# Optimization experiments

Measured on AMD Instinct MI355X. Metric: run time of the kernel, lower is better.

## Reference

```python
import jax, jax.numpy as jnp
import numpy as np

V, D, N, S = 100000, 256, 8192, 20
H = D  # hidden size == feat_dim (nn.LSTM(feat_dim, feat_dim))


def setup_inputs() -> dict:
    key = jax.random.key(0)
    ks = jax.random.split(key, 8)
    sc = 1.0 / np.sqrt(H)  # PyTorch LSTM default init scale
    return {
        "emb": jax.random.normal(ks[0], (V, D), jnp.float32),
        "w_ih_f": jax.random.normal(ks[1], (4 * H, D), jnp.float32) * sc,
        "w_hh_f": jax.random.normal(ks[2], (4 * H, H), jnp.float32) * sc,
        "b_f": jax.random.normal(ks[3], (4 * H,), jnp.float32) * sc,
        "w_ih_b": jax.random.normal(ks[4], (4 * H, D), jnp.float32) * sc,
        "w_hh_b": jax.random.normal(ks[5], (4 * H, H), jnp.float32) * sc,
        "b_b": jax.random.normal(ks[6], (4 * H,), jnp.float32) * sc,
        "neigh_idx": jax.random.randint(ks[7], (N, S), 0, V, dtype=jnp.int64),
    }


def _lstm_dir(x, w_ih, w_hh, b):
    """Batched unidirectional LSTM. x: [N, S, D] -> hidden states [N, S, H].
    PyTorch gate order: i, f, g, o."""
    h_dim = w_hh.shape[1]
    # precompute input contribution for all steps: [N, S, 4H]
    xg = jnp.einsum('nsd,gd->nsg', x, w_ih) + b

    def step(carry, xt):
        h, c = carry
        g = xt + h @ w_hh.T
        i, f, gg, o = jnp.split(g, 4, axis=-1)
        c = jax.nn.sigmoid(f) * c + jax.nn.sigmoid(i) * jnp.tanh(gg)
        h = jax.nn.sigmoid(o) * jnp.tanh(c)
        return (h, c), h

    n = x.shape[0]
    init = (jnp.zeros((n, h_dim), x.dtype), jnp.zeros((n, h_dim), x.dtype))
    _, hs = jax.lax.scan(step, init, jnp.swapaxes(xg, 0, 1))  # [S, N, H]
    return jnp.swapaxes(hs, 0, 1)


def reference(emb, w_ih_f, w_hh_f, b_f, w_ih_b, w_hh_b, b_b, neigh_idx):
    x = emb[neigh_idx]  # gather neighbor embeddings: [N, S, D]
    hf = _lstm_dir(x, w_ih_f, w_hh_f, b_f)                      # [N, S, H]
    hb = _lstm_dir(x[:, ::-1, :], w_ih_b, w_hh_b, b_b)[:, ::-1, :]
    h = jnp.concatenate([hf, hb], axis=-1)  # [N, S, 2H]
    summed = h.sum(axis=1)                  # sum over time: [N, 2H]
    # faithful to original: torch.mean over the 1-D summed vector -> scalar
    # broadcast into the full output row
    row = summed.mean(axis=-1, keepdims=True)  # [N, 1]
    return jnp.broadcast_to(row, summed.shape)  # [N, 2H]
```

## Files before the change

### kernel.cpp

```cpp
#include <hip/hip_runtime.h>

#define NN 8192
#define SS 20
#define DD 256
#define RGATE 1024
#define KKD 512

typedef __attribute__((ext_vector_type(8))) short short8;
typedef __attribute__((ext_vector_type(4))) float f32x4;

__device__ __forceinline__ unsigned short f2bf(float f) {
    unsigned int u = __float_as_uint(f);
    u += 0x7FFFu + ((u >> 16) & 1u);
    return (unsigned short)(u >> 16);
}

__device__ __forceinline__ void async_copy16(const void* g, void* l) {
    __builtin_amdgcn_global_load_lds(
        (const __attribute__((address_space(1))) void*)g,
        (__attribute__((address_space(3))) void*)l, 16, 0, 0);
}

__device__ __forceinline__ float sigm(float x) { return 1.0f / (1.0f + __expf(-x)); }
__device__ __forceinline__ float tanh_(float x) { return 2.0f / (1.0f + __expf(-2.0f * x)) - 1.0f; }

__global__ void convert_w(const float* __restrict__ wihf, const float* __restrict__ whhf,
                          const float* __restrict__ bf,   const float* __restrict__ wihb,
                          const float* __restrict__ whhb, const float* __restrict__ bb,
                          unsigned short* __restrict__ Wcat, float* __restrict__ bperm) {
    const int idx = blockIdx.x * 256 + threadIdx.x;
    const int dir = idx >> 19;
    const int rem = idx & ((1 << 19) - 1);
    const int rp  = rem >> 9;
    const int k   = rem & 511;
    const int j   = rp >> 2, gi = rp & 3;
    const int r   = gi * 256 + j;
    const float* wih = dir ? wihb : wihf;
    const float* whh = dir ? whhb : whhf;
    const float v = (k < 256) ? wih[r * 256 + k] : whh[r * 256 + (k - 256)];
    Wcat[idx] = f2bf(v);
    if (k == 0) {
        const float* b = dir ? bb : bf;
        bperm[dir * 1024 + rp] = b[r];
    }
}

__global__ __launch_bounds__(256) void gather_x(const float* __restrict__ emb,
                                                const int* __restrict__ idx,
                                                unsigned short* __restrict__ X) {
    const int w = threadIdx.x >> 6, lane = threadIdx.x & 63;
    #pragma unroll 4
    for (int i = 0; i < 16; ++i) {
        const int rid = (blockIdx.x * 16 + i) * 4 + w;
        const int n = rid / SS, t = rid - n * SS;
        const int row = idx[rid];
        const float4 v = ((const float4*)(emb + (size_t)row * DD))[lane];
        ushort4 o;
        o.x = f2bf(v.x); o.y = f2bf(v.y); o.z = f2bf(v.z); o.w = f2bf(v.w);
        ((ushort4*)(X + ((size_t)t * NN + n) * DD))[lane] = o;
    }
}

template <bool FIRST>
__global__ __launch_bounds__(512, 2) void lstm_step(
    const unsigned short* __restrict__ X,
    const unsigned short* __restrict__ Wcat,
    const float* __restrict__ bperm,
    unsigned short* __restrict__ hping,
    float* __restrict__ cstate,
    float* __restrict__ hsum,
    int s) {
    constexpr int NR = FIRST ? 8 : 16;
    const int b     = blockIdx.x;
    const int dir   = b & 1;
    const int nblk  = (b >> 3) & 3;
    const int mslab = (((b & 7) >> 1) << 3) | (b >> 5);
    const int m0    = mslab * 256;
    const int n0    = nblk * 256;

    const int t = dir ? (SS - 1 - s) : s;
    const unsigned short* Xt    = X + (size_t)t * NN * DD;
    const unsigned short* hprev = hping + ((size_t)((s & 1) * 2 + dir)) * NN * 256;
    unsigned short*       hnext = hping + ((size_t)((((s + 1) & 1) * 2) + dir)) * NN * 256;
    const unsigned short* W     = Wcat + (size_t)dir * RGATE * KKD;
    const float*          bp    = bperm + dir * RGATE;
    float*                cdir  = cstate + (size_t)dir * NN * 256;

    __shared__ __align__(16) char smem[98304];

    const int tid  = threadIdx.x;
    const int lane = tid & 63;
    const int w    = tid >> 6;
    const int wm   = w >> 1, wn = w & 1;
    const int quad = lane >> 4, l15 = lane & 15;
    const int jq   = lane & 3,  rl  = lane >> 2;

    const int srow  = lane >> 2;
    const int gsegl = (lane & 3) ^ ((lane >> 3) & 3);

    auto stage = [&](int rr, int buf) {
        const int k0 = (rr & 7) * 32;
        const unsigned short* Asrc = (rr < 8) ? Xt : hprev;
        char* Ad = smem + buf * 16384;
        char* Bd = smem + 49152 + buf * 16384;
        #pragma unroll
        for (int i = 0; i < 2; ++i) {
            const int lr = w * 32 + i * 16 + srow;
            async_copy16(Asrc + (size_t)(m0 + lr) * DD + k0 + gsegl * 8,
                         (void*)(Ad + (w * 32 + i * 16) * 64));
            async_copy16(W + (size_t)(n0 + lr) * KKD + rr * 32 + gsegl * 8,
                         (void*)(Bd + (w * 32 + i * 16) * 64));
        }
    };

    f32x4 acc[4][8];
    #pragma unroll
    for (int i = 0; i < 4; ++i)
        #pragma unroll
        for (int j = 0; j < 8; ++j) acc[i][j] = f32x4{0.f, 0.f, 0.f, 0.f};

    const int sA = (quad ^ ((l15 >> 1) & 3)) * 16;

    auto krnd = [&](int cb) {
        const char* Ab = smem + cb * 16384;
        const char* Bb = smem + 49152 + cb * 16384;
        short8 af[4], bfr[8];
        #pragma unroll
        for (int mt = 0; mt < 4; ++mt)
            af[mt] = *(const short8*)(Ab + (wm * 64 + mt * 16 + l15) * 64 + sA);
        #pragma unroll
        for (int nt = 0; nt < 8; ++nt)
            bfr[nt] = *(const short8*)(Bb + (wn * 128 + nt * 16 + l15) * 64 + sA);
        #pragma unroll
        for (int mt = 0; mt < 4; ++mt)
            #pragma unroll
            for (int nt = 0; nt < 8; ++nt)
                acc[mt][nt] = __builtin_amdgcn_mfma_f32_16x16x32_bf16(
                    af[mt], bfr[nt], acc[mt][nt], 0, 0, 0);
    };

    stage(0, 0);
    stage(1, 1);
    #pragma unroll
    for (int r = 0; r < NR - 2; ++r) {
        asm volatile("s_waitcnt vmcnt(4)" ::: "memory");
        asm volatile("s_barrier" ::: "memory");
        stage(r + 2, (r + 2) % 3);
        krnd(r % 3);
    }
    asm volatile("s_waitcnt vmcnt(4)" ::: "memory");
    asm volatile("s_barrier" ::: "memory");
    krnd((NR - 2) % 3);
    asm volatile("s_waitcnt vmcnt(0)" ::: "memory");
    asm volatile("s_barrier" ::: "memory");
    krnd((NR - 1) % 3);
    asm volatile("s_barrier" ::: "memory");

    float* my = (float*)smem + w * 1088;
    float hs[4] = {0.f, 0.f, 0.f, 0.f};

    #pragma unroll
    for (int half = 0; half < 2; ++half) {
        const int j0 = nblk * 64 + wn * 32 + half * 16 + jq * 4;
        f32x4 bias4[4];
        #pragma unroll
        for (int jj = 0; jj < 4; ++jj)
            bias4[jj] = *(const f32x4*)(bp + 4 * (j0 + jj));
        #pragma unroll
        for (int mt = 0; mt < 4; ++mt) {
            #pragma unroll
            for (int nt = 0; nt < 4; ++nt) {
                const int ntg = half * 4 + nt;
                #pragma unroll
                for (int v = 0; v < 4; ++v)
                    my[(quad * 4 + v) * 68 + nt * 16 + l15] = acc[mt][ntg][v];
            }
            asm volatile("s_waitcnt lgkmcnt(0)" ::: "memory");
            const int mg = m0 + wm * 64 + mt * 16 + rl;
            float* cptr = cdir + (size_t)mg * 256 + j0;
            f32x4 cold;
            if constexpr (!FIRST) cold = *(const f32x4*)cptr;
            else                  cold = f32x4{0.f, 0.f, 0.f, 0.f};
            f32x4 cnew;
            ushort4 hp;
            float lsum = 0.f;
            #pragma unroll
            for (int jj = 0; jj < 4; ++jj) {
                f32x4 g  = *(const f32x4*)(my + rl * 68 + (jq * 4 + jj) * 4);
                f32x4 bb = bias4[jj];
                const float gi = sigm(g.x + bb.x);
                const float gf = sigm(g.y + bb.y);
                const float gg = tanh_(g.z + bb.z);
                const float go = sigm(g.w + bb.w);
                const float cn = gf * cold[jj] + gi * gg;
                cnew[jj] = cn;
                const float hv = go * tanh_(cn);
                lsum += hv;
                ((unsigned short*)&hp)[jj] = f2bf(hv);
            }
            *(f32x4*)cptr = cnew;
            *(ushort4*)(hnext + (size_t)mg * 256 + j0) = hp;
            hs[mt] += lsum;
        }
    }

    #pragma unroll
    for (int mt = 0; mt < 4; ++mt) {
        float v = hs[mt];
        v += __shfl_xor(v, 1);
        v += __shfl_xor(v, 2);
        if (jq == 0) atomicAdd(&hsum[m0 + wm * 64 + mt * 16 + rl], v);
    }
}

__global__ void bcast_out(const float* __restrict__ hsum, float* __restrict__ out) {
    const int n = blockIdx.x;
    const float v = hsum[n] * (1.0f / 512.0f);
    float2 p; p.x = v; p.y = v;
    ((float2*)(out + (size_t)n * 512))[threadIdx.x] = p;
}

extern "C" void kernel_launch(void* const* d_in, const int* in_sizes, int n_in,
                              void* d_out, int out_size, void* d_ws, size_t ws_size,
                              hipStream_t stream) {
    const float* emb  = (const float*)d_in[0];
    const float* wihf = (const float*)d_in[1];
    const float* whhf = (const float*)d_in[2];
    const float* bf   = (const float*)d_in[3];
    const float* wihb = (const float*)d_in[4];
    const float* whhb = (const float*)d_in[5];
    const float* bb   = (const float*)d_in[6];
    const int*   idx  = (const int*)d_in[7];
    float* out = (float*)d_out;

    char* ws = (char*)d_ws;
    unsigned short* X     = (unsigned short*)(ws);
    unsigned short* Wcat  = (unsigned short*)(ws + 83886080);
    float*          bperm = (float*)(ws + 85983232);
    unsigned short* hping = (unsigned short*)(ws + 85991424);
    float*          cst   = (float*)(ws + 102768640);
    float*          hsum  = (float*)(ws + 119545856);

    hipMemsetAsync(hsum, 0, 32768, stream);

    convert_w<<<4096, 256, 0, stream>>>(wihf, whhf, bf, wihb, whhb, bb, Wcat, bperm);
    gather_x<<<2560, 256, 0, stream>>>(emb, idx, X);
    lstm_step<true><<<256, 512, 0, stream>>>(X, Wcat, bperm, hping, cst, hsum, 0);
    for (int s = 1; s < SS; ++s)
        lstm_step<false><<<256, 512, 0, stream>>>(X, Wcat, bperm, hping, cst, hsum, s);
    bcast_out<<<NN, 256, 0, stream>>>(hsum, out);
}
```

Before: 790.4 us.

## Restructure LSTM step GEMM main loop into double-buffered 64-wide K tiles with ping-pong scheduling

Replaces the 3-stage 32-wide K pipeline with a double-buffered 64-wide K tile staged in two halves. The wave layout changes from 4x2 to 2x4, so each wave now computes 128x64 instead of 64x128. The loop interleaves LDS fragment loads and async global-to-LDS copies between barrier-separated MFMA clusters, using setprio and sched_barrier so waves overlap memory with compute. LDS use rises to 128 KB. With __launch_bounds__(512,2) still in place, that may limit the kernel to one block per CU, and the extra barriers add synchronisation overhead.

Result: faster. 767.3 us (-2.9%).

```diff
diff --git a/kernel.cpp b/kernel.cpp
--- a/kernel.cpp
+++ b/kernel.cpp
@@ -70,7 +70,7 @@
     float* __restrict__ cstate,
     float* __restrict__ hsum,
     int s) {
-    constexpr int NR = FIRST ? 8 : 16;
+    constexpr int KT = FIRST ? 4 : 8;
     const int b     = blockIdx.x;
     const int dir   = b & 1;
     const int nblk  = (b >> 3) & 3;
@@ -86,130 +86,187 @@
     const float*          bp    = bperm + dir * RGATE;
     float*                cdir  = cstate + (size_t)dir * NN * 256;
 
-    __shared__ __align__(16) char smem[98304];
+    __shared__ __align__(16) char smem[131072];
 
     const int tid  = threadIdx.x;
     const int lane = tid & 63;
     const int w    = tid >> 6;
-    const int wm   = w >> 1, wn = w & 1;
+    const int wm   = w >> 2, wn = w & 3;
     const int quad = lane >> 4, l15 = lane & 15;
     const int jq   = lane & 3,  rl  = lane >> 2;
 
-    const int srow  = lane >> 2;
-    const int gsegl = (lane & 3) ^ ((lane >> 3) & 3);
-
-    auto stage = [&](int rr, int buf) {
-        const int k0 = (rr & 7) * 32;
-        const unsigned short* Asrc = (rr < 8) ? Xt : hprev;
-        char* Ad = smem + buf * 16384;
-        char* Bd = smem + 49152 + buf * 16384;
+    const int sr   = tid >> 3;
+    const int ss   = tid & 7;
+    const int wofs = w * 1024;
+    char* const ldsA = smem;
+    char* const ldsB = smem + 65536;
+
+    auto stA = [&](int kt, int h, int nb) {
+        const unsigned short* src; int col;
+        if (FIRST || kt < 4) { src = Xt;    col = kt * 64; }
+        else                 { src = hprev; col = (kt - 4) * 64; }
+        char* d = ldsA + nb * 32768 + h * 16384 + wofs;
         #pragma unroll
         for (int i = 0; i < 2; ++i) {
-            const int lr = w * 32 + i * 16 + srow;
-            async_copy16(Asrc + (size_t)(m0 + lr) * DD + k0 + gsegl * 8,
-                         (void*)(Ad + (w * 32 + i * 16) * 64));
-            async_copy16(W + (size_t)(n0 + lr) * KKD + rr * 32 + gsegl * 8,
-                         (void*)(Bd + (w * 32 + i * 16) * 64));
+            const int prow = h * 128 + i * 64 + sr;
+            const int gseg = ss ^ (prow & 7);
+            async_copy16(src + (size_t)(m0 + prow) * DD + col + gseg * 8,
+                         (void*)(d + i * 8192));
         }
     };
-
-    f32x4 acc[4][8];
-    #pragma unroll
-    for (int i = 0; i < 4; ++i)
-        #pragma unroll
-        for (int j = 0; j < 8; ++j) acc[i][j] = f32x4{0.f, 0.f, 0.f, 0.f};
-
-    const int sA = (quad ^ ((l15 >> 1) & 3)) * 16;
-
-    auto krnd = [&](int cb) {
-        const char* Ab = smem + cb * 16384;
-        const char* Bb = smem + 49152 + cb * 16384;
-        short8 af[4], bfr[8];
-        #pragma unroll
-        for (int mt = 0; mt < 4; ++mt)
-            af[mt] = *(const short8*)(Ab + (wm * 64 + mt * 16 + l15) * 64 + sA);
-        #pragma unroll
-        for (int nt = 0; nt < 8; ++nt)
-            bfr[nt] = *(const short8*)(Bb + (wn * 128 + nt * 16 + l15) * 64 + sA);
-        #pragma unroll
-        for (int mt = 0; mt < 4; ++mt)
-            #pragma unroll
-            for (int nt = 0; nt < 8; ++nt)
-                acc[mt][nt] = __builtin_amdgcn_mfma_f32_16x16x32_bf16(
-                    af[mt], bfr[nt], acc[mt][nt], 0, 0, 0);
+    auto stB = [&](int kt, int h, int nb) {
+        char* d = ldsB + nb * 32768 + h * 16384 + wofs;
+        #pragma unroll
+        for (int i = 0; i < 2; ++i) {
+            const int prow = h * 128 + i * 64 + sr;
+            const int gseg = ss ^ (prow & 7);
+            async_copy16(W + (size_t)(n0 + prow) * KKD + kt * 64 + gseg * 8,
+                         (void*)(d + i * 8192));
+        }
     };
 
-    stage(0, 0);
-    stage(1, 1);
-    #pragma unroll
-    for (int r = 0; r < NR - 2; ++r) {
-        asm volatile("s_waitcnt vmcnt(4)" ::: "memory");
-        asm volatile("s_barrier" ::: "memory");
-        stage(r + 2, (r + 2) % 3);
-        krnd(r % 3);
-    }
-    asm volatile("s_waitcnt vmcnt(4)" ::: "memory");
-    asm volatile("s_barrier" ::: "memory");
-    krnd((NR - 2) % 3);
+    const int axr   = l15 & 7;
+    const int aoffk[2] = { (wm * 128 + l15) * 128 + ((quad    ) ^ axr) * 16,
+                           (wm * 128 + l15) * 128 + ((quad + 4) ^ axr) * 16 };
+    const int boffk[2] = { (wn *  64 + l15) * 128 + ((quad    ) ^ axr) * 16,
+                           (wn *  64 + l15) * 128 + ((quad + 4) ^ axr) * 16 };
+
+    f32x4 acc[8][4];
+    #pragma unroll
+    for (int i = 0; i < 8; ++i)
+        #pragma unroll
+        for (int j = 0; j < 4; ++j) acc[i][j] = f32x4{0.f, 0.f, 0.f, 0.f};
+
+    auto ldA4 = [&](short8* dst, int mb, int kk, int bt) {
+        const char* base = ldsA + bt * 32768;
+        #pragma unroll
+        for (int i = 0; i < 4; ++i)
+            dst[i] = *(const short8*)(base + aoffk[kk] + (mb + i) * 2048);
+    };
+    auto ldB4 = [&](short8* dst, int kk, int bt) {
+        const char* base = ldsB + bt * 32768;
+        #pragma unroll
+        for (int i = 0; i < 4; ++i)
+            dst[i] = *(const short8*)(base + boffk[kk] + i * 2048);
+    };
+
+    stA(0, 0, 0); stA(0, 1, 0); stB(0, 0, 0); stB(0, 1, 0);
     asm volatile("s_waitcnt vmcnt(0)" ::: "memory");
     asm volatile("s_barrier" ::: "memory");
-    krnd((NR - 1) % 3);
-    asm volatile("s_barrier" ::: "memory");
+
+    #pragma unroll
+    for (int kt = 0; kt < KT; ++kt) {
+        const int bt = kt & 1, nb = bt ^ 1;
+        short8 a0[4], a1[4], b0[4];
+        ldA4(a0, 0, 0, bt); ldB4(b0, 0, bt);
+        if (kt + 1 < KT) { stA(kt + 1, 0, nb); stB(kt + 1, 0, nb); }
+        asm volatile("s_barrier" ::: "memory");
+        asm volatile("s_waitcnt lgkmcnt(0)" ::: "memory");
+        __builtin_amdgcn_sched_barrier(0);
+        __builtin_amdgcn_s_setprio(1);
+        #pragma unroll
+        for (int i = 0; i < 4; ++i)
+            #pragma unroll
+            for (int j = 0; j < 4; ++j)
+                acc[i][j] = __builtin_amdgcn_mfma_f32_16x16x32_bf16(
+                    a0[i], b0[j], acc[i][j], 0, 0, 0);
+        __builtin_amdgcn_s_setprio(0);
+        asm volatile("s_barrier" ::: "memory");
+        ldA4(a1, 4, 0, bt);
+        if (kt + 1 < KT) { stA(kt + 1, 1, nb); stB(kt + 1, 1, nb); }
+        asm volatile("s_barrier" ::: "memory");
+        asm volatile("s_waitcnt lgkmcnt(0)" ::: "memory");
+        __builtin_amdgcn_sched_barrier(0);
+        __builtin_amdgcn_s_setprio(1);
+        #pragma unroll
+        for (int i = 0; i < 4; ++i)
+            #pragma unroll
+            for (int j = 0; j < 4; ++j)
+                acc[4 + i][j] = __builtin_amdgcn_mfma_f32_16x16x32_bf16(
+                    a1[i], b0[j], acc[4 + i][j], 0, 0, 0);
+        __builtin_amdgcn_s_setprio(0);
+        asm volatile("s_barrier" ::: "memory");
+        ldA4(a0, 0, 1, bt); ldB4(b0, 1, bt);
+        asm volatile("s_barrier" ::: "memory");
+        asm volatile("s_waitcnt lgkmcnt(0)" ::: "memory");
+        __builtin_amdgcn_sched_barrier(0);
+        __builtin_amdgcn_s_setprio(1);
+        #pragma unroll
+        for (int i = 0; i < 4; ++i)
+            #pragma unroll
+            for (int j = 0; j < 4; ++j)
+                acc[i][j] = __builtin_amdgcn_mfma_f32_16x16x32_bf16(
+                    a0[i], b0[j], acc[i][j], 0, 0, 0);
+        __builtin_amdgcn_s_setprio(0);
+        asm volatile("s_barrier" ::: "memory");
+        ldA4(a1, 4, 1, bt);
+        asm volatile("s_barrier" ::: "memory");
+        asm volatile("s_waitcnt lgkmcnt(0)" ::: "memory");
+        __builtin_amdgcn_sched_barrier(0);
+        __builtin_amdgcn_s_setprio(1);
+        #pragma unroll
+        for (int i = 0; i < 4; ++i)
+            #pragma unroll
+            for (int j = 0; j < 4; ++j)
+                acc[4 + i][j] = __builtin_amdgcn_mfma_f32_16x16x32_bf16(
+                    a1[i], b0[j], acc[4 + i][j], 0, 0, 0);
+        __builtin_amdgcn_s_setprio(0);
+        if (kt + 1 < KT)
+            asm volatile("s_waitcnt vmcnt(0)" ::: "memory");
+        asm volatile("s_barrier" ::: "memory");
+    }
 
     float* my = (float*)smem + w * 1088;
-    float hs[4] = {0.f, 0.f, 0.f, 0.f};
-
-    #pragma unroll
-    for (int half = 0; half < 2; ++half) {
-        const int j0 = nblk * 64 + wn * 32 + half * 16 + jq * 4;
-        f32x4 bias4[4];
-        #pragma unroll
-        for (int jj = 0; jj < 4; ++jj)
-            bias4[jj] = *(const f32x4*)(bp + 4 * (j0 + jj));
-        #pragma unroll
-        for (int mt = 0; mt < 4; ++mt) {
-            #pragma unroll
-            for (int nt = 0; nt < 4; ++nt) {
-                const int ntg = half * 4 + nt;
-                #pragma unroll
-                for (int v = 0; v < 4; ++v)
-                    my[(quad * 4 + v) * 68 + nt * 16 + l15] = acc[mt][ntg][v];
-            }
-            asm volatile("s_waitcnt lgkmcnt(0)" ::: "memory");
-            const int mg = m0 + wm * 64 + mt * 16 + rl;
-            float* cptr = cdir + (size_t)mg * 256 + j0;
-            f32x4 cold;
-            if constexpr (!FIRST) cold = *(const f32x4*)cptr;
-            else                  cold = f32x4{0.f, 0.f, 0.f, 0.f};
-            f32x4 cnew;
-            ushort4 hp;
-            float lsum = 0.f;
-            #pragma unroll
-            for (int jj = 0; jj < 4; ++jj) {
-                f32x4 g  = *(const f32x4*)(my + rl * 68 + (jq * 4 + jj) * 4);
-                f32x4 bb = bias4[jj];
-                const float gi = sigm(g.x + bb.x);
-                const float gf = sigm(g.y + bb.y);
-                const float gg = tanh_(g.z + bb.z);
-                const float go = sigm(g.w + bb.w);
-                const float cn = gf * cold[jj] + gi * gg;
-                cnew[jj] = cn;
-                const float hv = go * tanh_(cn);
-                lsum += hv;
-                ((unsigned short*)&hp)[jj] = f2bf(hv);
-            }
-            *(f32x4*)cptr = cnew;
-            *(ushort4*)(hnext + (size_t)mg * 256 + j0) = hp;
-            hs[mt] += lsum;
+    const int j0 = nblk * 64 + wn * 16 + jq * 4;
+    f32x4 bias4[4];
+    #pragma unroll
+    for (int jj = 0; jj < 4; ++jj)
+        bias4[jj] = *(const f32x4*)(bp + 4 * (j0 + jj));
+    float hs[8];
+    #pragma unroll
+    for (int i = 0; i < 8; ++i) hs[i] = 0.f;
+
+    #pragma unroll
+    for (int mt = 0; mt < 8; ++mt) {
+        #pragma unroll
+        for (int nt = 0; nt < 4; ++nt)
+            #pragma unroll
+            for (int v = 0; v < 4; ++v)
+                my[(quad * 4 + v) * 68 + nt * 16 + l15] = acc[mt][nt][v];
+        asm volatile("s_waitcnt lgkmcnt(0)" ::: "memory");
+        const int mg = m0 + wm * 128 + mt * 16 + rl;
+        float* cptr = cdir + (size_t)mg * 256 + j0;
+        f32x4 cold;
+        if constexpr (!FIRST) cold = *(const f32x4*)cptr;
+        else                  cold = f32x4{0.f, 0.f, 0.f, 0.f};
+        f32x4 cnew;
+        ushort4 hp;
+        float lsum = 0.f;
+        #pragma unroll
+        for (int jj = 0; jj < 4; ++jj) {
+            f32x4 g  = *(const f32x4*)(my + rl * 68 + (jq * 4 + jj) * 4);
+            f32x4 bb = bias4[jj];
+            const float gi = sigm(g.x + bb.x);
+            const float gf = sigm(g.y + bb.y);
+            const float gg = tanh_(g.z + bb.z);
+            const float go = sigm(g.w + bb.w);
+            const float cn = gf * cold[jj] + gi * gg;
+            cnew[jj] = cn;
+            const float hv = go * tanh_(cn);
+            lsum += hv;
+            ((unsigned short*)&hp)[jj] = f2bf(hv);
         }
-    }
-
-    #pragma unroll
-    for (int mt = 0; mt < 4; ++mt) {
+        *(f32x4*)cptr = cnew;
+        *(ushort4*)(hnext + (size_t)mg * 256 + j0) = hp;
+        hs[mt] = lsum;
+    }
+
+    #pragma unroll
+    for (int mt = 0; mt < 8; ++mt) {
         float v = hs[mt];
         v += __shfl_xor(v, 1);
         v += __shfl_xor(v, 2);
-        if (jq == 0) atomicAdd(&hsum[m0 + wm * 64 + mt * 16 + rl], v);
+        if (jq == 0) atomicAdd(&hsum[m0 + wm * 128 + mt * 16 + rl], v);
     }
 }
 
```
